# Kernel optimization log

Measured on AMD Instinct MI355X. Metric: run time of the kernel, lower is better.

The kernel has to match this reference:

```python
import jax, jax.numpy as jnp
import numpy as np

B, D, N, DM, V = 1024, 256, 256, 128, 512  # batch, dsym, nrole/max_len, dmorphosyn, affix vocab


def setup_inputs() -> dict:
    key = jax.random.key(0)
    ks = jax.random.split(key, 8)
    return {
        "stem_form": jax.random.normal(ks[0], (B, D, N), jnp.float32),
        "morphosyn": jax.random.normal(ks[1], (B, DM), jnp.float32),
        "pivot_logits": jax.random.normal(ks[2], (2, 2, B, 5, N), jnp.float32),
        "W_affix": jax.random.normal(ks[3], (DM, V), jnp.float32) / np.sqrt(DM).astype(np.float32),
        "affix_vocab": jax.random.normal(ks[4], (V, D, N), jnp.float32),
        "alpha": jax.random.normal(ks[5], (2,), jnp.float32),
        "beta": jax.random.normal(ks[6], (2,), jnp.float32),
        "phi": jax.random.normal(ks[7], (5,), jnp.float32),
        "max_len": N,
    }


def reference(stem_form, morphosyn, pivot_logits, W_affix, affix_vocab, alpha, beta, phi, max_len):
    # mixture weights over 2 directions x 2 locations x 5 features
    a = jax.nn.softmax(alpha, -1)   # [2]
    b = jax.nn.softmax(beta, -1)    # [2]
    f = jax.nn.softmax(phi, -1)     # [5]
    # AffixVocab: morphosyntactic attention over affix vocabulary -> affix form
    attn = jax.nn.softmax(morphosyn @ W_affix, -1)            # [B, V]
    affix_form = jnp.einsum('bv,vdn->bdn', attn, affix_vocab)  # [B, D, N]
    # pivoter: soft one-hot pivot distributions over positions
    pivots = jax.nn.softmax(pivot_logits, -1)                  # [2, 2, B, 5, N]
    C = jnp.cumsum(pivots, -1)                                 # cumulative pivot mass
    # fused triple loop: sum_{drn,loc,ftr} alpha*beta*phi * morph_op(stem, affix, pivot)
    # morph_op = soft splice: keep stem before pivot, write affix after pivot.
    # Since morph_op is affine in C, the weighted sum collapses onto a single mask.
    wC = jnp.einsum('i,j,k,ijbkn->bn', a, b, f, C)[:, None, :]  # [B, 1, N]
    out_form = stem_form * (1.0 - wC) + affix_form * wC          # [B, D, N]
    return out_form
```

## Files before the change

### kernel.cpp

```cpp
#include <hip/hip_runtime.h>
#include <hip/hip_bf16.h>
#include <stdint.h>

typedef __bf16 bf16x8 __attribute__((ext_vector_type(8)));
typedef float f32x4 __attribute__((ext_vector_type(4)));

static __device__ __forceinline__ unsigned short f2bf(float x) {
    union { float f; unsigned u; } v; v.f = x;
    unsigned r = v.u + 0x7FFFu + ((v.u >> 16) & 1u);
    return (unsigned short)(r >> 16);
}

static __device__ __forceinline__ void gload_lds16(const void* g, void* l) {
    auto gp = (const unsigned int __attribute__((address_space(1)))*)(reinterpret_cast<uintptr_t>(g));
    auto lp = (unsigned int __attribute__((address_space(3)))*)(reinterpret_cast<uintptr_t>(l));
    __builtin_amdgcn_global_load_lds(gp, lp, 16, 0, 0);
}

__global__ __launch_bounds__(256, 4) void prepass_kernel(
        const float* __restrict__ vocab, unsigned short* __restrict__ Bt,
        const float* __restrict__ logits, const float* __restrict__ alpha,
        const float* __restrict__ beta, const float* __restrict__ phi,
        float* __restrict__ wC,
        const float* __restrict__ morphosyn, const float* __restrict__ W,
        unsigned short* __restrict__ attn_sw) {
    const int bid = blockIdx.x;
    const int t = threadIdx.x;
    const int lane = t & 63, wid = t >> 6;

    if (bid < 2048) {
        const int n0 = bid * 32;
        __shared__ unsigned int T[32 * 256];
        #pragma unroll
        for (int it = 0; it < 8; ++it) {
            int p = it * 256 + t;
            int v = (p >> 3) * 2;
            int col8 = p & 7;
            const float* g0 = vocab + (size_t)v * 65536 + n0 + col8 * 4;
            float4 a = *(const float4*)g0;
            float4 c = *(const float4*)(g0 + 65536);
            #pragma unroll
            for (int j = 0; j < 4; ++j) {
                int n = col8 * 4 + j;
                unsigned d = (unsigned)f2bf((&a.x)[j]) | ((unsigned)f2bf((&c.x)[j]) << 16);
                T[n * 256 + (v >> 1)] = d;
            }
        }
        __syncthreads();
        #pragma unroll
        for (int it = 0; it < 8; ++it) {
            int qq = it * 256 + t;
            int r = qq >> 6, c = qq & 63;
            int swz = ((n0 + r) >> 2) & 3;
            int dc = (c & ~3) | ((c & 3) ^ swz);
            uint4 d = *(const uint4*)(&T[r * 256 + c * 4]);
            *(uint4*)(Bt + (size_t)(n0 + r) * 512 + dc * 8) = d;
        }
    } else if (bid < 3072) {
        const int b = bid - 2048;
        __shared__ float part[4][256];
        __shared__ float wsum[4];

        float a0 = alpha[0], a1 = alpha[1];
        float am = fmaxf(a0, a1);
        float ea0 = __expf(a0 - am), ea1 = __expf(a1 - am);
        float as = ea0 + ea1;
        float b0 = beta[0], b1 = beta[1];
        float bm = fmaxf(b0, b1);
        float eb0 = __expf(b0 - bm), eb1 = __expf(b1 - bm);
        float bs = eb0 + eb1;
        float p[5];
        float pm = -1e30f;
        #pragma unroll
        for (int k = 0; k < 5; ++k) { p[k] = phi[k]; pm = fmaxf(pm, p[k]); }
        float ps = 0.f;
        #pragma unroll
        for (int k = 0; k < 5; ++k) { p[k] = __expf(p[k] - pm); ps += p[k]; }
        const float wa[2] = {ea0 / as, ea1 / as}, wb[2] = {eb0 / bs, eb1 / bs};

        f32x4 accv = {0.f, 0.f, 0.f, 0.f};
        #pragma unroll
        for (int s5 = 0; s5 < 5; ++s5) {
            int sl = wid * 5 + s5;
            int i = sl >= 10;
            int j = (sl / 5) & 1;
            int k = sl - (sl / 5) * 5;
            const float* base = logits + ((size_t)(((i * 2 + j) * 1024 + b) * 5 + k)) * 256;
            f32x4 x = *(const f32x4*)(base + lane * 4);
            float mx = fmaxf(fmaxf(x[0], x[1]), fmaxf(x[2], x[3]));
            #pragma unroll
            for (int o = 32; o; o >>= 1) mx = fmaxf(mx, __shfl_xor(mx, o));
            f32x4 e;
            float sm = 0.f;
            #pragma unroll
            for (int r = 0; r < 4; ++r) { e[r] = __expf(x[r] - mx); sm += e[r]; }
            #pragma unroll
            for (int o = 32; o; o >>= 1) sm += __shfl_xor(sm, o);
            float w = wa[i] * wb[j] * (p[k] / ps) / sm;
            #pragma unroll
            for (int r = 0; r < 4; ++r) accv[r] += w * e[r];
        }
        *(f32x4*)&part[wid][lane * 4] = accv;
        __syncthreads();
        float v = part[0][t] + part[1][t] + part[2][t] + part[3][t];
        #pragma unroll
        for (int o = 1; o < 64; o <<= 1) {
            float u = __shfl_up(v, o);
            if (lane >= o) v += u;
        }
        if (lane == 63) wsum[wid] = v;
        __syncthreads();
        float offv = 0.f;
        for (int w2 = 0; w2 < wid; ++w2) offv += wsum[w2];
        wC[b * 256 + t] = v + offv;
    } else {
        const int b = bid - 3072;
        __shared__ float ms[128];
        __shared__ float red[4];
        if (t < 128) ms[t] = morphosyn[b * 128 + t];
        __syncthreads();
        float acc0 = 0.f, acc1 = 0.f;
        #pragma unroll 8
        for (int dm = 0; dm < 128; ++dm) {
            float m = ms[dm];
            acc0 = fmaf(m, W[dm * 512 + t], acc0);
            acc1 = fmaf(m, W[dm * 512 + t + 256], acc1);
        }
        float mx = fmaxf(acc0, acc1);
        #pragma unroll
        for (int o = 32; o; o >>= 1) mx = fmaxf(mx, __shfl_xor(mx, o));
        if (lane == 0) red[wid] = mx;
        __syncthreads();
        mx = fmaxf(fmaxf(red[0], red[1]), fmaxf(red[2], red[3]));
        __syncthreads();
        float e0 = __expf(acc0 - mx), e1 = __expf(acc1 - mx);
        float sm = e0 + e1;
        #pragma unroll
        for (int o = 32; o; o >>= 1) sm += __shfl_xor(sm, o);
        if (lane == 0) red[wid] = sm;
        __syncthreads();
        sm = red[0] + red[1] + red[2] + red[3];
        const float inv = 1.0f / sm;
        const int swz = (b >> 2) & 3;
        #pragma unroll
        for (int h = 0; h < 2; ++h) {
            int v = t + h * 256;
            int ae = (v >> 5) * 32 + ((((v >> 3) & 3) ^ swz) << 3) + (v & 7);
            attn_sw[b * 512 + ae] = f2bf((h ? e1 : e0) * inv);
        }
    }
}

__global__ __launch_bounds__(512, 4) void gemm_kernel(
        const unsigned short* __restrict__ attn_sw,
        const unsigned short* __restrict__ Bt,
        const float* __restrict__ stem,
        const float* __restrict__ wC,
        float* __restrict__ out) {
    const int bid = blockIdx.x;
    const int xcd = bid & 7, s = bid >> 3;
    const int m0 = (s & 3) << 8;
    const int n0 = ((xcd << 6) + (s >> 2)) << 7;
    const int t = threadIdx.x;
    const int lane = t & 63, wid = t >> 6;
    const int wr = wid >> 1, wcn = wid & 1;
    const int q = lane >> 4, rl = lane & 15;
    const int soff = ((q ^ ((rl >> 2) & 3)) << 4);

    __shared__ __align__(16) unsigned short ldsb[40960];

    f32x4 acc[4][4];
    const f32x4 z = {0.f, 0.f, 0.f, 0.f};
    #pragma unroll
    for (int i = 0; i < 4; ++i)
        #pragma unroll
        for (int j = 0; j < 4; ++j) acc[i][j] = z;

    const unsigned short* a_src = attn_sw + (size_t)(m0 + (t >> 2)) * 512 + (t & 3) * 8;
    const unsigned short* b_src = Bt + (size_t)(n0 + (t >> 2)) * 512 + (t & 3) * 8;

#define STAGE_A(kt) do { \
    unsigned short* dst_ = ldsb + ((kt) % 3) * 8192; \
    const int ko_ = (kt) * 32; \
    gload_lds16(a_src + ko_, dst_ + t * 8); \
    gload_lds16(a_src + 65536 + ko_, dst_ + 4096 + t * 8); \
} while (0)

#define STAGE_B(kt) do { \
    unsigned short* dst_ = ldsb + 24576 + ((kt) % 4) * 4096; \
    gload_lds16(b_src + (kt) * 32, dst_ + t * 8); \
} while (0)

#define KSTEP(kt, SA, SB, VMSTR) do { \
    asm volatile("s_waitcnt vmcnt(" VMSTR ")" ::: "memory"); \
    __builtin_amdgcn_s_barrier(); \
    __builtin_amdgcn_sched_barrier(0); \
    if (SA) STAGE_A((kt) + 2); \
    if (SB) STAGE_B((kt) + 3); \
    const char* abase_ = (const char*)(ldsb + ((kt) % 3) * 8192); \
    const char* bbase_ = (const char*)(ldsb + 24576 + ((kt) % 4) * 4096); \
    bf16x8 af_[4], bfv_[4]; \
    _Pragma("unroll") \
    for (int f_ = 0; f_ < 4; ++f_) \
        af_[f_] = *(const bf16x8*)(abase_ + (wr * 64 + f_ * 16 + rl) * 64 + soff); \
    _Pragma("unroll") \
    for (int j_ = 0; j_ < 4; ++j_) \
        bfv_[j_] = *(const bf16x8*)(bbase_ + (wcn * 64 + j_ * 16 + rl) * 64 + soff); \
    __builtin_amdgcn_s_setprio(1); \
    _Pragma("unroll") \
    for (int fm_ = 0; fm_ < 4; ++fm_) \
        _Pragma("unroll") \
        for (int j_ = 0; j_ < 4; ++j_) \
            acc[fm_][j_] = __builtin_amdgcn_mfma_f32_16x16x32_bf16( \
                af_[fm_], bfv_[j_], acc[fm_][j_], 0, 0, 0); \
    __builtin_amdgcn_s_setprio(0); \
    __builtin_amdgcn_sched_barrier(0); \
} while (0)

    STAGE_B(0); STAGE_A(0); STAGE_B(1); STAGE_A(1); STAGE_B(2);
    KSTEP(0, 1, 1, "4");  KSTEP(1, 1, 1, "4");  KSTEP(2, 1, 1, "4");  KSTEP(3, 1, 1, "4");
    KSTEP(4, 1, 1, "4");  KSTEP(5, 1, 1, "4");  KSTEP(6, 1, 1, "4");  KSTEP(7, 1, 1, "4");
    KSTEP(8, 1, 1, "4");  KSTEP(9, 1, 1, "4");  KSTEP(10, 1, 1, "4"); KSTEP(11, 1, 1, "4");
    KSTEP(12, 1, 1, "4"); KSTEP(13, 1, 0, "4"); KSTEP(14, 0, 0, "3"); KSTEP(15, 0, 0, "0");
#undef STAGE_A
#undef STAGE_B
#undef KSTEP

    float* cs = (float*)ldsb;
    const int erow = t >> 5;
    const int ecol = (t & 31) * 4;
    #pragma unroll
    for (int sb = 0; sb < 4; ++sb) {
        f32x4 sv[4];
        #pragma unroll
        for (int i2 = 0; i2 < 4; ++i2) {
            int b = m0 + sb * 64 + i2 * 16 + erow;
            sv[i2] = *(const f32x4*)&stem[(size_t)b * 65536 + (size_t)n0 + ecol];
        }
        __syncthreads();
        if (wr == sb) {
            #pragma unroll
            for (int fm = 0; fm < 4; ++fm) {
                #pragma unroll
                for (int n = 0; n < 4; ++n) {
                    int c = wcn * 64 + n * 16 + rl;
                    #pragma unroll
                    for (int i = 0; i < 4; ++i)
                        cs[(fm * 16 + q * 4 + i) * 132 + c] = acc[fm][n][i];
                }
            }
        }
        __syncthreads();
        #pragma unroll
        for (int i2 = 0; i2 < 4; ++i2) {
            int row = i2 * 16 + erow;
            int b = m0 + sb * 64 + row;
            size_t gb = (size_t)b * 65536 + (size_t)n0 + ecol;
            f32x4 cv = *(const f32x4*)&cs[row * 132 + ecol];
            f32x4 wv = *(const f32x4*)&wC[((size_t)b << 8) + (n0 & 255) + ecol];
            f32x4 ov;
            #pragma unroll
            for (int jj = 0; jj < 4; ++jj)
                ov[jj] = sv[i2][jj] + (cv[jj] - sv[i2][jj]) * wv[jj];
            *(f32x4*)&out[gb] = ov;
        }
    }
}

__global__ void gemm_fb(const unsigned short* __restrict__ attn_sw,
                        const float* __restrict__ vocab,
                        const float* __restrict__ stem,
                        const float* __restrict__ wC,
                        float* __restrict__ out) {
    const int tile_m = blockIdx.x & 7;
    const int tile_n = blockIdx.x >> 3;
    const int m0 = tile_m << 7;
    const int n0 = tile_n << 7;
    const int t = threadIdx.x;
    const int lane = t & 63;
    const int wv = t >> 6;
    const int wm = wv >> 1, wn = wv & 1;

    __shared__ unsigned short Asl[128 * 32];
    __shared__ unsigned short Bsl[128 * 32];

    f32x4 acc[4][4];
    const f32x4 z = {0.f, 0.f, 0.f, 0.f};
    #pragma unroll
    for (int i = 0; i < 4; ++i)
        #pragma unroll
        for (int j = 0; j < 4; ++j) acc[i][j] = z;

    const unsigned short* a_base = attn_sw + ((size_t)m0 << 9);
    const int q = lane >> 4;
    const int rl = lane & 15;

    for (int ks = 0; ks < 16; ++ks) {
        #pragma unroll
        for (int it = 0; it < 2; ++it) {
            int idx = it * 256 + t;
            int r = idx >> 2, blk = idx & 3;
            gload_lds16(a_base + r * 512 + ks * 32 + blk * 8, Asl + idx * 8);
        }
        #pragma unroll
        for (int it = 0; it < 2; ++it) {
            int lin = it * 256 + t;
            int pair = lin >> 5;
            int chunk = lin & 31;
            int k = pair * 2;
            const float* g0 = vocab + (size_t)(ks * 32 + k) * 65536 + n0 + chunk * 4;
            float4 v0 = *(const float4*)g0;
            float4 v1 = *(const float4*)(g0 + 65536);
            #pragma unroll
            for (int j = 0; j < 4; ++j) {
                int n = chunk * 4 + j;
                unsigned d = (unsigned)f2bf((&v0.x)[j]) | ((unsigned)f2bf((&v1.x)[j]) << 16);
                int ae = n * 32 + ((((k >> 3) ^ ((n >> 2) & 3))) << 3) + (k & 7);
                *(unsigned*)((char*)Bsl + ae * 2) = d;
            }
        }
        __syncthreads();
        bf16x8 af[4], bfr[4];
        #pragma unroll
        for (int f = 0; f < 4; ++f) {
            int r = wm * 64 + f * 16 + rl;
            af[f] = *(const bf16x8*)((const char*)Asl + r * 64 + ((q ^ ((r >> 2) & 3)) << 4));
            int c = wn * 64 + f * 16 + rl;
            bfr[f] = *(const bf16x8*)((const char*)Bsl + c * 64 + ((q ^ ((c >> 2) & 3)) << 4));
        }
        __syncthreads();
        #pragma unroll
        for (int fm = 0; fm < 4; ++fm)
            #pragma unroll
            for (int fn = 0; fn < 4; ++fn)
                acc[fm][fn] = __builtin_amdgcn_mfma_f32_16x16x32_bf16(af[fm], bfr[fn], acc[fm][fn], 0, 0, 0);
    }

    #pragma unroll
    for (int fm = 0; fm < 4; ++fm) {
        int rbase = m0 + wm * 64 + fm * 16 + ((lane >> 4) << 2);
        #pragma unroll
        for (int fn = 0; fn < 4; ++fn) {
            int c = n0 + wn * 64 + fn * 16 + (lane & 15);
            #pragma unroll
            for (int i = 0; i < 4; ++i) {
                int b = rbase + i;
                float w = wC[(b << 8) + (c & 255)];
                size_t o = ((size_t)b << 16) + (size_t)c;
                float sv = stem[o];
                out[o] = sv + (acc[fm][fn][i] - sv) * w;
            }
        }
    }
}

__global__ void attn_kernel(const float* __restrict__ morphosyn,
                            const float* __restrict__ W,
                            unsigned short* __restrict__ attn_sw) {
    const int b = blockIdx.x;
    const int t = threadIdx.x;
    __shared__ float ms[128];
    __shared__ float red[4];
    if (t < 128) ms[t] = morphosyn[b * 128 + t];
    __syncthreads();
    float acc0 = 0.f, acc1 = 0.f;
    #pragma unroll 8
    for (int dm = 0; dm < 128; ++dm) {
        float m = ms[dm];
        acc0 = fmaf(m, W[dm * 512 + t], acc0);
        acc1 = fmaf(m, W[dm * 512 + t + 256], acc1);
    }
    const int lane = t & 63, wid = t >> 6;
    float mx = fmaxf(acc0, acc1);
    #pragma unroll
    for (int o = 32; o; o >>= 1) mx = fmaxf(mx, __shfl_xor(mx, o));
    if (lane == 0) red[wid] = mx;
    __syncthreads();
    mx = fmaxf(fmaxf(red[0], red[1]), fmaxf(red[2], red[3]));
    __syncthreads();
    float e0 = __expf(acc0 - mx), e1 = __expf(acc1 - mx);
    float sm = e0 + e1;
    #pragma unroll
    for (int o = 32; o; o >>= 1) sm += __shfl_xor(sm, o);
    if (lane == 0) red[wid] = sm;
    __syncthreads();
    sm = red[0] + red[1] + red[2] + red[3];
    const float inv = 1.0f / sm;
    const int swz = (b >> 2) & 3;
    #pragma unroll
    for (int h = 0; h < 2; ++h) {
        int v = t + h * 256;
        int ae = (v >> 5) * 32 + ((((v >> 3) & 3) ^ swz) << 3) + (v & 7);
        attn_sw[b * 512 + ae] = f2bf((h ? e1 : e0) * inv);
    }
}

__global__ void wc_kernel(const float* __restrict__ logits,
                          const float* __restrict__ alpha,
                          const float* __restrict__ beta,
                          const float* __restrict__ phi,
                          float* __restrict__ wC) {
    const int b = blockIdx.x;
    const int t = threadIdx.x;
    const int lane = t & 63, wid = t >> 6;
    __shared__ float part[4][256];
    __shared__ float wsum[4];
    float a0 = alpha[0], a1 = alpha[1];
    float am = fmaxf(a0, a1);
    float ea0 = __expf(a0 - am), ea1 = __expf(a1 - am);
    float as = ea0 + ea1;
    float b0 = beta[0], b1 = beta[1];
    float bm = fmaxf(b0, b1);
    float eb0 = __expf(b0 - bm), eb1 = __expf(b1 - bm);
    float bs = eb0 + eb1;
    float p[5];
    float pm = -1e30f;
    #pragma unroll
    for (int k = 0; k < 5; ++k) { p[k] = phi[k]; pm = fmaxf(pm, p[k]); }
    float ps = 0.f;
    #pragma unroll
    for (int k = 0; k < 5; ++k) { p[k] = __expf(p[k] - pm); ps += p[k]; }
    const float wa[2] = {ea0 / as, ea1 / as}, wb[2] = {eb0 / bs, eb1 / bs};
    f32x4 accv = {0.f, 0.f, 0.f, 0.f};
    #pragma unroll
    for (int s5 = 0; s5 < 5; ++s5) {
        int sl = wid * 5 + s5;
        int i = sl >= 10;
        int j = (sl / 5) & 1;
        int k = sl - (sl / 5) * 5;
        const float* base = logits + ((size_t)(((i * 2 + j) * 1024 + b) * 5 + k)) * 256;
        f32x4 x = *(const f32x4*)(base + lane * 4);
        float mx = fmaxf(fmaxf(x[0], x[1]), fmaxf(x[2], x[3]));
        #pragma unroll
        for (int o = 32; o; o >>= 1) mx = fmaxf(mx, __shfl_xor(mx, o));
        f32x4 e;
        float sm = 0.f;
        #pragma unroll
        for (int r = 0; r < 4; ++r) { e[r] = __expf(x[r] - mx); sm += e[r]; }
        #pragma unroll
        for (int o = 32; o; o >>= 1) sm += __shfl_xor(sm, o);
        float w = wa[i] * wb[j] * (p[k] / ps) / sm;
        #pragma unroll
        for (int r = 0; r < 4; ++r) accv[r] += w * e[r];
    }
    *(f32x4*)&part[wid][lane * 4] = accv;
    __syncthreads();
    float v = part[0][t] + part[1][t] + part[2][t] + part[3][t];
    #pragma unroll
    for (int o = 1; o < 64; o <<= 1) {
        float u = __shfl_up(v, o);
        if (lane >= o) v += u;
    }
    if (lane == 63) wsum[wid] = v;
    __syncthreads();
    float offv = 0.f;
    for (int w2 = 0; w2 < wid; ++w2) offv += wsum[w2];
    wC[b * 256 + t] = v + offv;
}

extern "C" void kernel_launch(void* const* d_in, const int* in_sizes, int n_in,
                              void* d_out, int out_size, void* d_ws, size_t ws_size,
                              hipStream_t stream) {
    const float* stem    = (const float*)d_in[0];
    const float* morpho  = (const float*)d_in[1];
    const float* logits  = (const float*)d_in[2];
    const float* W       = (const float*)d_in[3];
    const float* vocab   = (const float*)d_in[4];
    const float* alpha   = (const float*)d_in[5];
    const float* beta    = (const float*)d_in[6];
    const float* phi     = (const float*)d_in[7];
    float* out = (float*)d_out;

    unsigned short* attn_sw = (unsigned short*)d_ws;
    float* wC = (float*)((char*)d_ws + (1 << 20));
    unsigned short* Bt = (unsigned short*)((char*)d_ws + (2 << 20));

    const size_t need = (size_t)(2 << 20) + (size_t)64 * 1024 * 1024;

    if (ws_size >= need) {
        prepass_kernel<<<4096, 256, 0, stream>>>(vocab, Bt, logits, alpha, beta, phi, wC,
                                                 morpho, W, attn_sw);
        gemm_kernel<<<2048, 512, 0, stream>>>(attn_sw, Bt, stem, wC, out);
    } else {
        attn_kernel<<<1024, 256, 0, stream>>>(morpho, W, attn_sw);
        wc_kernel<<<1024, 256, 0, stream>>>(logits, alpha, beta, phi, wC);
        gemm_fb<<<4096, 256, 0, stream>>>(attn_sw, vocab, stem, wC, out);
    }
}
```

Before: 215.7 us.

## Double-buffer stem tiles into LDS asynchronously during GEMM epilogue

```diff
diff --git a/kernel.cpp b/kernel.cpp
--- a/kernel.cpp
+++ b/kernel.cpp
@@ -226,45 +226,74 @@
 #undef STAGE_B
 #undef KSTEP
 
-    float* cs = (float*)ldsb;
+    float* cs = (float*)(ldsb + 32768);
     const int erow = t >> 5;
     const int ecol = (t & 31) * 4;
-    #pragma unroll
-    for (int sb = 0; sb < 4; ++sb) {
-        f32x4 sv[4];
-        #pragma unroll
-        for (int i2 = 0; i2 < 4; ++i2) {
-            int b = m0 + sb * 64 + i2 * 16 + erow;
-            sv[i2] = *(const f32x4*)&stem[(size_t)b * 65536 + (size_t)n0 + ecol];
-        }
-        __syncthreads();
-        if (wr == sb) {
-            #pragma unroll
-            for (int fm = 0; fm < 4; ++fm) {
-                #pragma unroll
-                for (int n = 0; n < 4; ++n) {
-                    int c = wcn * 64 + n * 16 + rl;
-                    #pragma unroll
-                    for (int i = 0; i < 4; ++i)
-                        cs[(fm * 16 + q * 4 + i) * 132 + c] = acc[fm][n][i];
-                }
-            }
-        }
-        __syncthreads();
-        #pragma unroll
-        for (int i2 = 0; i2 < 4; ++i2) {
-            int row = i2 * 16 + erow;
-            int b = m0 + sb * 64 + row;
-            size_t gb = (size_t)b * 65536 + (size_t)n0 + ecol;
-            f32x4 cv = *(const f32x4*)&cs[row * 132 + ecol];
-            f32x4 wv = *(const f32x4*)&wC[((size_t)b << 8) + (n0 & 255) + ecol];
-            f32x4 ov;
-            #pragma unroll
-            for (int jj = 0; jj < 4; ++jj)
-                ov[jj] = sv[i2][jj] + (cv[jj] - sv[i2][jj]) * wv[jj];
-            *(f32x4*)&out[gb] = ov;
-        }
-    }
+
+#define EBAR() do { \
+    asm volatile("s_waitcnt lgkmcnt(0)" ::: "memory"); \
+    __builtin_amdgcn_s_barrier(); \
+    __builtin_amdgcn_sched_barrier(0); \
+} while (0)
+
+#define SISSUE(p) do { \
+    unsigned short* d_ = ldsb + ((p) & 1) * 16384; \
+    const float* g_ = stem + (size_t)(m0 + (p) * 64 + erow) * 65536 + n0 + (t & 31) * 4; \
+    _Pragma("unroll") \
+    for (int k_ = 0; k_ < 4; ++k_) \
+        gload_lds16(g_ + (size_t)(k_ * 16) * 65536, d_ + k_ * 4096 + t * 8); \
+} while (0)
+
+#define EHALF(sb, h, TB) do { \
+    if (wr == (sb)) { \
+        _Pragma("unroll") \
+        for (int fmr_ = 0; fmr_ < 2; ++fmr_) { \
+            _Pragma("unroll") \
+            for (int n_ = 0; n_ < 4; ++n_) \
+                _Pragma("unroll") \
+                for (int i_ = 0; i_ < 4; ++i_) \
+                    cs[(fmr_ * 16 + q * 4 + i_) * 128 + wcn * 64 + n_ * 16 + rl] = \
+                        acc[(h) * 2 + fmr_][n_][i_]; \
+        } \
+    } \
+    EBAR(); \
+    _Pragma("unroll") \
+    for (int j2_ = 0; j2_ < 2; ++j2_) { \
+        int row_ = ((h) * 2 + j2_) * 16 + erow; \
+        int b_ = m0 + (sb) * 64 + row_; \
+        size_t gb_ = (size_t)b_ * 65536 + (size_t)n0 + ecol; \
+        f32x4 cv_ = *(const f32x4*)&cs[(j2_ * 16 + erow) * 128 + ecol]; \
+        f32x4 sv_ = *(const f32x4*)((const char*)(ldsb + ((sb) & 1) * 16384) + \
+                                    (size_t)row_ * 512 + (t & 31) * 16); \
+        f32x4 wv_ = *(const f32x4*)&wC[((size_t)b_ << 8) + (n0 & 255) + ecol]; \
+        f32x4 ov_; \
+        _Pragma("unroll") \
+        for (int jj_ = 0; jj_ < 4; ++jj_) \
+            ov_[jj_] = sv_[jj_] + (cv_[jj_] - sv_[jj_]) * wv_[jj_]; \
+        *(f32x4*)&out[gb_] = ov_; \
+    } \
+    if (TB) EBAR(); \
+} while (0)
+
+#define EPASS(sb, DOISS) do { \
+    asm volatile("s_waitcnt vmcnt(4) lgkmcnt(0)" ::: "memory"); \
+    __builtin_amdgcn_s_barrier(); \
+    __builtin_amdgcn_sched_barrier(0); \
+    if (DOISS) SISSUE((sb) + 1); \
+    EHALF(sb, 0, 1); \
+    EHALF(sb, 1, 0); \
+} while (0)
+
+    EBAR();
+    SISSUE(0); SISSUE(1);
+    EPASS(0, 0);
+    EPASS(1, 1);
+    EPASS(2, 1);
+    EPASS(3, 0);
+#undef EBAR
+#undef SISSUE
+#undef EHALF
+#undef EPASS
 }
 
 __global__ void gemm_fb(const unsigned short* __restrict__ attn_sw,
```

New measurement: 225.7 us. 4.7% more time.
